# Kernel optimization log

Hardware: AMD Instinct MI355X
Metric: run time of the kernel (lower is better)

Reference implementation:

```python
import jax, jax.numpy as jnp
from jax import lax
import numpy as np

B, W, F, D = 48, 8192, 64, 128  # batch, input_window, c_in, d_model


def setup_inputs() -> dict:
    key = jax.random.key(0)
    k0, k1, k2, k3 = jax.random.split(key, 4)
    x = jax.random.normal(k0, (B, W, F), jnp.float32)
    # ContextConv(c_in->c_in, k=3): conv1d over time, zero 'same' padding (repo layer, assumed standard conv)
    ctx_w = jax.random.normal(k1, (F, F, 3), jnp.float32) * (2.0 / (F * 3)) ** 0.5
    ctx_b = jnp.zeros((F,), jnp.float32)
    # tokenConv: Conv1d(c_in -> d_model, k=3, circular padding, no bias), kaiming fan_in
    token_w = jax.random.normal(k2, (D, F, 3), jnp.float32) * (2.0 / (F * 3)) ** 0.5
    # seW: Linear(c_in -> input_window)
    seW_w = jax.random.normal(k3, (W, F), jnp.float32) * (1.0 / F) ** 0.5
    seW_b = jnp.zeros((W,), jnp.float32)
    return dict(x=x, ctx_w=ctx_w, ctx_b=ctx_b, token_w=token_w, seW_w=seW_w, seW_b=seW_b)


def _conv1d_ncw(x_ncw, w_oiw, padding):
    return lax.conv_general_dilated(
        x_ncw, w_oiw, window_strides=(1,), padding=padding,
        dimension_numbers=("NCW", "OIW", "NCW"))


def reference(x, ctx_w, ctx_b, token_w, seW_w, seW_b):
    # ---- contextConv: (B,W,F) -> (B,W,F), conv over time ----
    xc = _conv1d_ncw(x.transpose(0, 2, 1), ctx_w, [(1, 1)])  # (B,F,W)
    xc = (xc + ctx_b[None, :, None]).transpose(0, 2, 1)       # (B,W,F)

    # ---- structure_embedding (src is detached in torch) ----
    src = lax.stop_gradient(x)
    srcn = src / jnp.linalg.norm(src, axis=-1, keepdims=True)         # row-normalize each timestep
    gram = jnp.einsum('bwf,bwg->bfg', srcn, srcn)                      # batched f x f matmul
    xse = jax.nn.relu(jnp.einsum('bfg,wg->bfw', gram, seW_w) + seW_b[None, None, :])  # (B,F,W)
    xse = xse.transpose(0, 2, 1)                                       # (B,W,F)

    # ---- tokenConv with circular padding ----
    h = (xc + xse).transpose(0, 2, 1)                                  # (B,F,W)
    hp = jnp.pad(h, ((0, 0), (0, 0), (1, 1)), mode='wrap')
    out = _conv1d_ncw(hp, token_w, 'VALID')                            # (B,D,W)
    return out.transpose(0, 2, 1)                                      # (B,W,D)
```

## Files before the change

kernel.cpp:

```cpp
#include <hip/hip_runtime.h>
#include <stdint.h>

#define Bb 48
#define Ww 8192
#define Ff 64
#define Dd 128
#define TWt 64
#define NSLAB 32

#define WS_GRAMP 0u
#define WS_GRAM  25165824u
#define WS_TWT   25952256u
#define WS_CWT   26001408u
#define WS_GBF   26025984u
#define WS_SWB   26419200u
#define WS_XBF   27467776u
#define WS_TOTAL (27467776ull + 50331648ull)

typedef __bf16 bf16x8 __attribute__((ext_vector_type(8)));
typedef float f32x4 __attribute__((ext_vector_type(4)));

__device__ __forceinline__ float bf2f(unsigned short u){
  union { unsigned int i; float f; } v; v.i = ((unsigned int)u) << 16; return v.f;
}
__device__ __forceinline__ unsigned short f2bf(float f){
  union { float f; unsigned int i; } v; v.f = f;
  unsigned int i = v.i;
  return (unsigned short)((i + 0x7fffu + ((i >> 16) & 1u)) >> 16);
}
__device__ __forceinline__ f32x4 mfma16(bf16x8 a, bf16x8 b, f32x4 c){
  return __builtin_amdgcn_mfma_f32_16x16x32_bf16(a, b, c, 0, 0, 0);
}

__device__ __forceinline__ int swz(int row, int col){
  return row * 64 + ((((col >> 3) ^ (row & 7))) << 3) + (col & 7);
}

__global__ __launch_bounds__(256) void prep_weights(const float* __restrict__ ctx_w,
                                                    const float* __restrict__ token_w,
                                                    const float* __restrict__ seW_w,
                                                    unsigned short* __restrict__ cwT,
                                                    unsigned short* __restrict__ twT,
                                                    unsigned short* __restrict__ sWb,
                                                    int fast)
{
  const int bx = blockIdx.x;
  if (bx < 144){
    int idx = bx * 256 + threadIdx.x;
    const int ntw = Dd * 192;
    if (idx < ntw){
      int d = idx / 192, kim = idx % 192;
      int ktap = kim >> 6, fi = kim & 63;
      twT[idx] = f2bf(token_w[(d * Ff + fi) * 3 + ktap]);
    } else if (idx < ntw + Ff * 192){
      int i2 = idx - ntw;
      int f = i2 / 192, kim = i2 % 192;
      int ktap = kim >> 6, fi = kim & 63;
      cwT[i2] = f2bf(ctx_w[(f * Ff + fi) * 3 + ktap]);
    }
  } else if (fast){
    int i = ((bx - 144) * 256 + threadIdx.x) * 8;
    float4 a0 = *(const float4*)(seW_w + i);
    float4 a1 = *(const float4*)(seW_w + i + 4);
    union { uint4 q; unsigned short s[8]; } u;
    u.s[0]=f2bf(a0.x); u.s[1]=f2bf(a0.y); u.s[2]=f2bf(a0.z); u.s[3]=f2bf(a0.w);
    u.s[4]=f2bf(a1.x); u.s[5]=f2bf(a1.y); u.s[6]=f2bf(a1.z); u.s[7]=f2bf(a1.w);
    *(uint4*)(sWb + i) = u.q;
  }
}

__global__ __launch_bounds__(256) void gram_kernel(const float* __restrict__ x,
                                                   unsigned short* __restrict__ xbf,
                                                   float* __restrict__ gramP,
                                                   int writeXbf)
{
  const int b = blockIdx.y;
  const int w_base = blockIdx.x * (Ww / NSLAB);
  const int t = threadIdx.x;
  const int lane = t & 63;
  const int wave = t >> 6;
  const int lrow = lane & 15;
  const int lk = lane >> 4;

  __shared__ unsigned short st[64 * 64];

  f32x4 acc[4] = {};

  const int wl = t >> 2;
  const int f0 = (t & 3) * 16;

  float v[16];
  {
    const float* xr = x + ((size_t)b * Ww + (size_t)(w_base + wl)) * Ff + f0;
    *(float4*)(v)      = *(const float4*)(xr);
    *(float4*)(v + 4)  = *(const float4*)(xr + 4);
    *(float4*)(v + 8)  = *(const float4*)(xr + 8);
    *(float4*)(v + 12) = *(const float4*)(xr + 12);
  }

  for (int sc = 0; sc < 4; ++sc) {
    const size_t rowg = (size_t)b * Ww + (size_t)(w_base + sc * 64 + wl);

    float ss = 0.f;
#pragma unroll
    for (int i = 0; i < 16; ++i) ss += v[i] * v[i];
    ss += __shfl_xor(ss, 1);
    ss += __shfl_xor(ss, 2);
    float rinv = rsqrtf(ss);

    union { uint4 q[2]; unsigned short s[16]; } u;
#pragma unroll
    for (int i = 0; i < 16; ++i){
      u.s[i] = f2bf(v[i]);
      st[swz(f0 + i, wl)] = f2bf(v[i] * rinv);
    }
    if (writeXbf){
      unsigned short* dst = xbf + rowg * Ff + f0;
      *(uint4*)(dst)     = u.q[0];
      *(uint4*)(dst + 8) = u.q[1];
    }

    float vn[16];
    if (sc < 3){
      const float* xr = x + ((size_t)b * Ww + (size_t)(w_base + (sc+1) * 64 + wl)) * Ff + f0;
      *(float4*)(vn)      = *(const float4*)(xr);
      *(float4*)(vn + 4)  = *(const float4*)(xr + 4);
      *(float4*)(vn + 8)  = *(const float4*)(xr + 8);
      *(float4*)(vn + 12) = *(const float4*)(xr + 12);
    }

    __syncthreads();
#pragma unroll
    for (int kc = 0; kc < 2; ++kc){
      const int kw = kc * 32 + lk * 8;
      bf16x8 bfr = *(const bf16x8*)(st + swz(wave * 16 + lrow, kw));
#pragma unroll
      for (int mt = 0; mt < 4; ++mt){
        bf16x8 af = *(const bf16x8*)(st + swz(mt * 16 + lrow, kw));
        acc[mt] = mfma16(af, bfr, acc[mt]);
      }
    }
    __syncthreads();

    if (sc < 3){
#pragma unroll
      for (int i = 0; i < 16; ++i) v[i] = vn[i];
    }
  }

  float* gb = gramP + ((size_t)(blockIdx.x * Bb + b)) * 4096;
#pragma unroll
  for (int mt = 0; mt < 4; ++mt)
#pragma unroll
    for (int r = 0; r < 4; ++r){
      int f = mt * 16 + lk * 4 + r;
      int g = wave * 16 + lrow;
      gb[f * 64 + g] = acc[mt][r];
    }
}

__global__ __launch_bounds__(256) void gram_reduce(const float* __restrict__ gramP,
                                                   float* __restrict__ gram,
                                                   unsigned short* __restrict__ gbf,
                                                   int fast)
{
  int i = blockIdx.x * 256 + threadIdx.x;
  int b = i >> 10;
  int q = i & 1023;
  float sx = 0.f, sy = 0.f, sz = 0.f, sw = 0.f;
#pragma unroll
  for (int sl = 0; sl < NSLAB; ++sl){
    const float4 v = *(const float4*)(gramP + (((size_t)(sl * Bb + b)) << 12) + q * 4);
    sx += v.x; sy += v.y; sz += v.z; sw += v.w;
  }
  float4 s = make_float4(sx, sy, sz, sw);
  *(float4*)(gram + (((size_t)b) << 12) + q * 4) = s;
  if (fast){
    union { unsigned long long u; unsigned short h[4]; } u;
    u.h[0] = f2bf(sx); u.h[1] = f2bf(sy); u.h[2] = f2bf(sz); u.h[3] = f2bf(sw);
    *(unsigned long long*)(gbf + (((size_t)b) << 12) + q * 4) = u.u;
  }
}

__global__ __launch_bounds__(256, 4) void fused_kernel(
    const float* __restrict__ x,
    const unsigned short* __restrict__ xbf,
    const float* __restrict__ ctx_b,
    const float* __restrict__ seW_w,
    const unsigned short* __restrict__ sWb,
    const float* __restrict__ seW_b,
    const float* __restrict__ gram,
    const unsigned short* __restrict__ gbf,
    const unsigned short* __restrict__ cwT,
    const unsigned short* __restrict__ twT,
    float* __restrict__ out,
    int fast)
{
  const int b = blockIdx.y;
  const int w0 = blockIdx.x * TWt;
  const int t = threadIdx.x;
  const int lane = t & 63;
  const int wave = t >> 6;
  const int lrow = lane & 15;
  const int lk = lane >> 4;

  __shared__ __align__(16) unsigned char smem[(84 + 80 + 66) * 64 * 2];
  unsigned short* xs  = (unsigned short*)smem;
  unsigned short* sws = xs + 84 * 64;
  unsigned short* hsh = sws + 80 * 64;

  if (fast){
    for (int item = t; item < 84 * 8; item += 256){
      int i = item >> 3, seg = item & 7;
      int c = w0 - 2 + i;
      uint4 val = make_uint4(0u,0u,0u,0u);
      if (c >= 0 && c < Ww) val = *(const uint4*)(xbf + ((size_t)b*Ww + c)*Ff + seg*8);
      *(uint4*)(xs + swz(i, seg*8)) = val;
    }
    for (int item = t; item < 80 * 8; item += 256){
      int i = item >> 3, seg = item & 7;
      int hc = (w0 - 1 + i) & (Ww - 1);
      *(uint4*)(sws + swz(i, seg*8)) = *(const uint4*)(sWb + (size_t)hc*Ff + seg*8);
    }
  } else {
    for (int item = t; item < 84 * 8; item += 256){
      int i = item >> 3, seg = item & 7;
      int c = w0 - 2 + i;
      union { uint4 q; unsigned short s[8]; } u;
      if (c >= 0 && c < Ww){
        const float* xr = x + ((size_t)b*Ww + c)*Ff + seg*8;
        float4 a0 = *(const float4*)(xr);
        float4 a1 = *(const float4*)(xr + 4);
        u.s[0]=f2bf(a0.x); u.s[1]=f2bf(a0.y); u.s[2]=f2bf(a0.z); u.s[3]=f2bf(a0.w);
        u.s[4]=f2bf(a1.x); u.s[5]=f2bf(a1.y); u.s[6]=f2bf(a1.z); u.s[7]=f2bf(a1.w);
      } else {
        u.q = make_uint4(0u,0u,0u,0u);
      }
      *(uint4*)(xs + swz(i, seg*8)) = u.q;
    }
  }
  __syncthreads();

  const int nt = wave;
  bf16x8 cw_frag[6];
  {
    const unsigned short* p = cwT + (nt*16 + lrow)*192 + lk*8;
#pragma unroll
    for (int kc = 0; kc < 6; ++kc) cw_frag[kc] = *(const bf16x8*)(p + kc*32);
  }
  bf16x8 se_frag[2];
  if (fast){
    const unsigned short* gp = gbf + (size_t)b*4096 + (nt*16 + lrow)*64;
#pragma unroll
    for (int kc = 0; kc < 2; ++kc) se_frag[kc] = *(const bf16x8*)(gp + kc*32 + lk*8);
  } else {
    const float* gb = gram + (size_t)b * 4096;
#pragma unroll
    for (int kc = 0; kc < 2; ++kc){
      union { bf16x8 v; unsigned short s[8]; } u;
#pragma unroll
      for (int j = 0; j < 8; ++j){
        int g = kc*32 + lk*8 + j;
        u.s[j] = f2bf(gb[g*64 + nt*16 + lrow]);
      }
      se_frag[kc] = u.v;
    }
  }

  f32x4 xc_acc[5] = {};
  f32x4 se_acc[5] = {};

#pragma unroll
  for (int mt = 0; mt < 5; ++mt){
#pragma unroll
    for (int kc = 0; kc < 6; ++kc){
      int kim = kc*32 + lk*8;
      int ktap = kim >> 6, fi = kim & 63;
      bf16x8 a = *(const bf16x8*)(xs + swz(mt*16 + lrow + ktap, fi));
      xc_acc[mt] = mfma16(a, cw_frag[kc], xc_acc[mt]);
    }
    if (fast){
#pragma unroll
      for (int kc = 0; kc < 2; ++kc){
        bf16x8 a = *(const bf16x8*)(sws + swz(mt*16 + lrow, kc*32 + lk*8));
        se_acc[mt] = mfma16(a, se_frag[kc], se_acc[mt]);
      }
    } else {
      int hc = (w0 - 1 + mt*16 + lrow) & (Ww - 1);
      const float* sp = seW_w + (size_t)hc * Ff;
#pragma unroll
      for (int kc = 0; kc < 2; ++kc){
        union { bf16x8 v; unsigned short s[8]; } u;
        float4 a0 = *(const float4*)(sp + kc*32 + lk*8);
        float4 a1 = *(const float4*)(sp + kc*32 + lk*8 + 4);
        u.s[0]=f2bf(a0.x); u.s[1]=f2bf(a0.y); u.s[2]=f2bf(a0.z); u.s[3]=f2bf(a0.w);
        u.s[4]=f2bf(a1.x); u.s[5]=f2bf(a1.y); u.s[6]=f2bf(a1.z); u.s[7]=f2bf(a1.w);
        se_acc[mt] = mfma16(u.v, se_frag[kc], se_acc[mt]);
      }
    }
  }

  {
    float cb = ctx_b[nt*16 + lrow];
#pragma unroll
    for (int mt = 0; mt < 5; ++mt){
#pragma unroll
      for (int r = 0; r < 4; ++r){
        int j = mt*16 + lk*4 + r;
        if (j < 66){
          int hc = (w0 - 1 + j) & (Ww - 1);
          float se = se_acc[mt][r] + seW_b[hc];
          se = se > 0.f ? se : 0.f;
          hsh[swz(j, nt*16 + lrow)] = f2bf(xc_acc[mt][r] + cb + se);
        }
      }
    }
  }
  __syncthreads();

  if (blockIdx.x == 0 || blockIdx.x == (Ww/TWt - 1)){
    const int j  = (blockIdx.x == 0) ? 0 : 65;
    const int hc = (blockIdx.x == 0) ? (Ww - 1) : 0;
    if (t < 64){
      const int f = t;
      float a = ctx_b[f];
      for (int ktap = 0; ktap < 3; ++ktap){
        int c = hc + ktap - 1;
        if (c >= 0 && c < Ww){
          const float* xr = x + ((size_t)b*Ww + c)*Ff;
          const unsigned short* wr = cwT + f*192 + ktap*64;
          for (int fi = 0; fi < 64; ++fi) a += xr[fi] * bf2f(wr[fi]);
        }
      }
      const float* gb = gram + (size_t)b * 4096;
      const float* sp = seW_w + (size_t)hc * Ff;
      float se = seW_b[hc];
      for (int g = 0; g < 64; ++g) se += sp[g] * gb[g*64 + f];
      se = se > 0.f ? se : 0.f;
      hsh[swz(j, f)] = f2bf(a + se);
    }
    __syncthreads();
  }

  bf16x8 tw_frag[2][6];
#pragma unroll
  for (int q = 0; q < 2; ++q){
    const unsigned short* p = twT + ((wave*2 + q)*16 + lrow)*192 + lk*8;
#pragma unroll
    for (int kc = 0; kc < 6; ++kc) tw_frag[q][kc] = *(const bf16x8*)(p + kc*32);
  }
  f32x4 oacc[4][2] = {};
#pragma unroll
  for (int mt = 0; mt < 4; ++mt){
#pragma unroll
    for (int kc = 0; kc < 6; ++kc){
      int kim = kc*32 + lk*8;
      int ktap = kim >> 6, fi = kim & 63;
      bf16x8 a = *(const bf16x8*)(hsh + swz(mt*16 + lrow + ktap, fi));
#pragma unroll
      for (int q = 0; q < 2; ++q)
        oacc[mt][q] = mfma16(a, tw_frag[q][kc], oacc[mt][q]);
    }
  }

#pragma unroll
  for (int mt = 0; mt < 4; ++mt){
#pragma unroll
    for (int q = 0; q < 2; ++q)
#pragma unroll
      for (int r = 0; r < 4; ++r){
        int row = w0 + mt*16 + lk*4 + r;
        int d   = (wave*2 + q)*16 + lrow;
        out[((size_t)b*Ww + row)*Dd + d] = oacc[mt][q][r];
      }
  }
}

extern "C" void kernel_launch(void* const* d_in, const int* in_sizes, int n_in,
                              void* d_out, int out_size, void* d_ws, size_t ws_size,
                              hipStream_t stream)
{
  const float* x       = (const float*)d_in[0];
  const float* ctx_w   = (const float*)d_in[1];
  const float* ctx_b   = (const float*)d_in[2];
  const float* token_w = (const float*)d_in[3];
  const float* seW_w   = (const float*)d_in[4];
  const float* seW_b   = (const float*)d_in[5];
  float* out = (float*)d_out;

  char* ws = (char*)d_ws;
  float*          gramP = (float*)(ws + WS_GRAMP);
  float*          gram  = (float*)(ws + WS_GRAM);
  unsigned short* twT   = (unsigned short*)(ws + WS_TWT);
  unsigned short* cwT   = (unsigned short*)(ws + WS_CWT);
  unsigned short* gbf   = (unsigned short*)(ws + WS_GBF);
  unsigned short* sWb   = (unsigned short*)(ws + WS_SWB);
  unsigned short* xbf   = (unsigned short*)(ws + WS_XBF);

  const int fast = (ws_size >= (size_t)WS_TOTAL) ? 1 : 0;

  prep_weights<<<dim3(400), dim3(256), 0, stream>>>(ctx_w, token_w, seW_w, cwT, twT, sWb, fast);
  gram_kernel<<<dim3(NSLAB, Bb), dim3(256), 0, stream>>>(x, xbf, gramP, fast);
  gram_reduce<<<dim3(192), dim3(256), 0, stream>>>(gramP, gram, gbf, fast);
  fused_kernel<<<dim3(Ww/TWt, Bb), dim3(256), 0, stream>>>(
      x, xbf, ctx_b, seW_w, sWb, seW_b, gram, gbf, cwT, twT, out, fast);
}
```

Measured before the change: 362.9 us.

## Process four time tiles per block with register prefetch of next tile

```diff
diff --git a/kernel.cpp b/kernel.cpp
--- a/kernel.cpp
+++ b/kernel.cpp
@@ -6,6 +6,7 @@
 #define Ff 64
 #define Dd 128
 #define TWt 64
+#define TPB 4
 #define NSLAB 32
 
 #define WS_GRAMP 0u
@@ -182,7 +183,7 @@
   }
 }
 
-__global__ __launch_bounds__(256, 4) void fused_kernel(
+__global__ __launch_bounds__(256, 3) void fused_kernel(
     const float* __restrict__ x,
     const unsigned short* __restrict__ xbf,
     const float* __restrict__ ctx_b,
@@ -197,57 +198,31 @@
     int fast)
 {
   const int b = blockIdx.y;
-  const int w0 = blockIdx.x * TWt;
   const int t = threadIdx.x;
   const int lane = t & 63;
   const int wave = t >> 6;
   const int lrow = lane & 15;
   const int lk = lane >> 4;
 
-  __shared__ __align__(16) unsigned char smem[(84 + 80 + 66) * 64 * 2];
-  unsigned short* xs  = (unsigned short*)smem;
-  unsigned short* sws = xs + 84 * 64;
-  unsigned short* hsh = sws + 80 * 64;
-
-  if (fast){
-    for (int item = t; item < 84 * 8; item += 256){
-      int i = item >> 3, seg = item & 7;
-      int c = w0 - 2 + i;
-      uint4 val = make_uint4(0u,0u,0u,0u);
-      if (c >= 0 && c < Ww) val = *(const uint4*)(xbf + ((size_t)b*Ww + c)*Ff + seg*8);
-      *(uint4*)(xs + swz(i, seg*8)) = val;
-    }
-    for (int item = t; item < 80 * 8; item += 256){
-      int i = item >> 3, seg = item & 7;
-      int hc = (w0 - 1 + i) & (Ww - 1);
-      *(uint4*)(sws + swz(i, seg*8)) = *(const uint4*)(sWb + (size_t)hc*Ff + seg*8);
-    }
-  } else {
-    for (int item = t; item < 84 * 8; item += 256){
-      int i = item >> 3, seg = item & 7;
-      int c = w0 - 2 + i;
-      union { uint4 q; unsigned short s[8]; } u;
-      if (c >= 0 && c < Ww){
-        const float* xr = x + ((size_t)b*Ww + c)*Ff + seg*8;
-        float4 a0 = *(const float4*)(xr);
-        float4 a1 = *(const float4*)(xr + 4);
-        u.s[0]=f2bf(a0.x); u.s[1]=f2bf(a0.y); u.s[2]=f2bf(a0.z); u.s[3]=f2bf(a0.w);
-        u.s[4]=f2bf(a1.x); u.s[5]=f2bf(a1.y); u.s[6]=f2bf(a1.z); u.s[7]=f2bf(a1.w);
-      } else {
-        u.q = make_uint4(0u,0u,0u,0u);
-      }
-      *(uint4*)(xs + swz(i, seg*8)) = u.q;
-    }
-  }
-  __syncthreads();
+  __shared__ __align__(16) unsigned short xs[84 * 64];
+  __shared__ __align__(16) unsigned short sws[80 * 64];
+  __shared__ __align__(16) unsigned short hsh[66 * 64];
 
   const int nt = wave;
+
   bf16x8 cw_frag[6];
   {
     const unsigned short* p = cwT + (nt*16 + lrow)*192 + lk*8;
 #pragma unroll
     for (int kc = 0; kc < 6; ++kc) cw_frag[kc] = *(const bf16x8*)(p + kc*32);
   }
+  bf16x8 tw_frag[2][6];
+#pragma unroll
+  for (int q = 0; q < 2; ++q){
+    const unsigned short* p = twT + ((wave*2 + q)*16 + lrow)*192 + lk*8;
+#pragma unroll
+    for (int kc = 0; kc < 6; ++kc) tw_frag[q][kc] = *(const bf16x8*)(p + kc*32);
+  }
   bf16x8 se_frag[2];
   if (fast){
     const unsigned short* gp = gbf + (size_t)b*4096 + (nt*16 + lrow)*64;
@@ -267,112 +242,174 @@
     }
   }
 
-  f32x4 xc_acc[5] = {};
-  f32x4 se_acc[5] = {};
-
-#pragma unroll
-  for (int mt = 0; mt < 5; ++mt){
-#pragma unroll
-    for (int kc = 0; kc < 6; ++kc){
-      int kim = kc*32 + lk*8;
-      int ktap = kim >> 6, fi = kim & 63;
-      bf16x8 a = *(const bf16x8*)(xs + swz(mt*16 + lrow + ktap, fi));
-      xc_acc[mt] = mfma16(a, cw_frag[kc], xc_acc[mt]);
-    }
+  const int w0 = blockIdx.x * (TWt * TPB);
+
+  uint4 xr[3], sr[3];
+  if (fast){
+#pragma unroll
+    for (int k = 0; k < 3; ++k){
+      int item = t + 256*k;
+      if (item < 84*8){
+        int i = item >> 3, seg = item & 7, c = w0 - 2 + i;
+        uint4 val = make_uint4(0u,0u,0u,0u);
+        if (c >= 0 && c < Ww) val = *(const uint4*)(xbf + ((size_t)b*Ww + c)*Ff + seg*8);
+        xr[k] = val;
+      }
+      if (item < 80*8){
+        int i = item >> 3, seg = item & 7, hc = (w0 - 1 + i) & (Ww - 1);
+        sr[k] = *(const uint4*)(sWb + (size_t)hc*Ff + seg*8);
+      }
+    }
+  }
+
+  for (int tt = 0; tt < TPB; ++tt){
+    const int wt = w0 + tt * TWt;
+
     if (fast){
 #pragma unroll
-      for (int kc = 0; kc < 2; ++kc){
-        bf16x8 a = *(const bf16x8*)(sws + swz(mt*16 + lrow, kc*32 + lk*8));
-        se_acc[mt] = mfma16(a, se_frag[kc], se_acc[mt]);
+      for (int k = 0; k < 3; ++k){
+        int item = t + 256*k;
+        if (item < 84*8){ int i = item >> 3, seg = item & 7; *(uint4*)(xs + swz(i, seg*8)) = xr[k]; }
+        if (item < 80*8){ int i = item >> 3, seg = item & 7; *(uint4*)(sws + swz(i, seg*8)) = sr[k]; }
       }
     } else {
-      int hc = (w0 - 1 + mt*16 + lrow) & (Ww - 1);
-      const float* sp = seW_w + (size_t)hc * Ff;
-#pragma unroll
-      for (int kc = 0; kc < 2; ++kc){
-        union { bf16x8 v; unsigned short s[8]; } u;
-        float4 a0 = *(const float4*)(sp + kc*32 + lk*8);
-        float4 a1 = *(const float4*)(sp + kc*32 + lk*8 + 4);
-        u.s[0]=f2bf(a0.x); u.s[1]=f2bf(a0.y); u.s[2]=f2bf(a0.z); u.s[3]=f2bf(a0.w);
-        u.s[4]=f2bf(a1.x); u.s[5]=f2bf(a1.y); u.s[6]=f2bf(a1.z); u.s[7]=f2bf(a1.w);
-        se_acc[mt] = mfma16(u.v, se_frag[kc], se_acc[mt]);
-      }
-    }
-  }
-
-  {
-    float cb = ctx_b[nt*16 + lrow];
+      for (int item = t; item < 84 * 8; item += 256){
+        int i = item >> 3, seg = item & 7;
+        int c = wt - 2 + i;
+        union { uint4 q; unsigned short s[8]; } u;
+        if (c >= 0 && c < Ww){
+          const float* xrp = x + ((size_t)b*Ww + c)*Ff + seg*8;
+          float4 a0 = *(const float4*)(xrp);
+          float4 a1 = *(const float4*)(xrp + 4);
+          u.s[0]=f2bf(a0.x); u.s[1]=f2bf(a0.y); u.s[2]=f2bf(a0.z); u.s[3]=f2bf(a0.w);
+          u.s[4]=f2bf(a1.x); u.s[5]=f2bf(a1.y); u.s[6]=f2bf(a1.z); u.s[7]=f2bf(a1.w);
+        } else {
+          u.q = make_uint4(0u,0u,0u,0u);
+        }
+        *(uint4*)(xs + swz(i, seg*8)) = u.q;
+      }
+    }
+    __syncthreads();
+
+    if (fast && tt + 1 < TPB){
+      const int wn = wt + TWt;
+#pragma unroll
+      for (int k = 0; k < 3; ++k){
+        int item = t + 256*k;
+        if (item < 84*8){
+          int i = item >> 3, seg = item & 7, c = wn - 2 + i;
+          uint4 val = make_uint4(0u,0u,0u,0u);
+          if (c >= 0 && c < Ww) val = *(const uint4*)(xbf + ((size_t)b*Ww + c)*Ff + seg*8);
+          xr[k] = val;
+        }
+        if (item < 80*8){
+          int i = item >> 3, seg = item & 7, hc = (wn - 1 + i) & (Ww - 1);
+          sr[k] = *(const uint4*)(sWb + (size_t)hc*Ff + seg*8);
+        }
+      }
+    }
+
+    f32x4 xc_acc[5] = {};
+    f32x4 se_acc[5] = {};
+
 #pragma unroll
     for (int mt = 0; mt < 5; ++mt){
 #pragma unroll
-      for (int r = 0; r < 4; ++r){
-        int j = mt*16 + lk*4 + r;
-        if (j < 66){
-          int hc = (w0 - 1 + j) & (Ww - 1);
-          float se = se_acc[mt][r] + seW_b[hc];
-          se = se > 0.f ? se : 0.f;
-          hsh[swz(j, nt*16 + lrow)] = f2bf(xc_acc[mt][r] + cb + se);
-        }
-      }
-    }
-  }
-  __syncthreads();
-
-  if (blockIdx.x == 0 || blockIdx.x == (Ww/TWt - 1)){
-    const int j  = (blockIdx.x == 0) ? 0 : 65;
-    const int hc = (blockIdx.x == 0) ? (Ww - 1) : 0;
-    if (t < 64){
-      const int f = t;
-      float a = ctx_b[f];
-      for (int ktap = 0; ktap < 3; ++ktap){
-        int c = hc + ktap - 1;
-        if (c >= 0 && c < Ww){
-          const float* xr = x + ((size_t)b*Ww + c)*Ff;
-          const unsigned short* wr = cwT + f*192 + ktap*64;
-          for (int fi = 0; fi < 64; ++fi) a += xr[fi] * bf2f(wr[fi]);
-        }
-      }
-      const float* gb = gram + (size_t)b * 4096;
-      const float* sp = seW_w + (size_t)hc * Ff;
-      float se = seW_b[hc];
-      for (int g = 0; g < 64; ++g) se += sp[g] * gb[g*64 + f];
-      se = se > 0.f ? se : 0.f;
-      hsh[swz(j, f)] = f2bf(a + se);
+      for (int kc = 0; kc < 6; ++kc){
+        int kim = kc*32 + lk*8;
+        int ktap = kim >> 6, fi = kim & 63;
+        bf16x8 a = *(const bf16x8*)(xs + swz(mt*16 + lrow + ktap, fi));
+        xc_acc[mt] = mfma16(a, cw_frag[kc], xc_acc[mt]);
+      }
+      if (fast){
+#pragma unroll
+        for (int kc = 0; kc < 2; ++kc){
+          bf16x8 a = *(const bf16x8*)(sws + swz(mt*16 + lrow, kc*32 + lk*8));
+          se_acc[mt] = mfma16(a, se_frag[kc], se_acc[mt]);
+        }
+      } else {
+        int hc = (wt - 1 + mt*16 + lrow) & (Ww - 1);
+        const float* sp = seW_w + (size_t)hc * Ff;
+#pragma unroll
+        for (int kc = 0; kc < 2; ++kc){
+          union { bf16x8 v; unsigned short s[8]; } u;
+          float4 a0 = *(const float4*)(sp + kc*32 + lk*8);
+          float4 a1 = *(const float4*)(sp + kc*32 + lk*8 + 4);
+          u.s[0]=f2bf(a0.x); u.s[1]=f2bf(a0.y); u.s[2]=f2bf(a0.z); u.s[3]=f2bf(a0.w);
+          u.s[4]=f2bf(a1.x); u.s[5]=f2bf(a1.y); u.s[6]=f2bf(a1.z); u.s[7]=f2bf(a1.w);
+          se_acc[mt] = mfma16(u.v, se_frag[kc], se_acc[mt]);
+        }
+      }
+    }
+
+    {
+      float cb = ctx_b[nt*16 + lrow];
+#pragma unroll
+      for (int mt = 0; mt < 5; ++mt){
+#pragma unroll
+        for (int r = 0; r < 4; ++r){
+          int j = mt*16 + lk*4 + r;
+          if (j < 66){
+            int hc = (wt - 1 + j) & (Ww - 1);
+            float se = se_acc[mt][r] + seW_b[hc];
+            se = se > 0.f ? se : 0.f;
+            hsh[swz(j, nt*16 + lrow)] = f2bf(xc_acc[mt][r] + cb + se);
+          }
+        }
+      }
     }
     __syncthreads();
-  }
-
-  bf16x8 tw_frag[2][6];
-#pragma unroll
-  for (int q = 0; q < 2; ++q){
-    const unsigned short* p = twT + ((wave*2 + q)*16 + lrow)*192 + lk*8;
-#pragma unroll
-    for (int kc = 0; kc < 6; ++kc) tw_frag[q][kc] = *(const bf16x8*)(p + kc*32);
-  }
-  f32x4 oacc[4][2] = {};
-#pragma unroll
-  for (int mt = 0; mt < 4; ++mt){
-#pragma unroll
-    for (int kc = 0; kc < 6; ++kc){
-      int kim = kc*32 + lk*8;
-      int ktap = kim >> 6, fi = kim & 63;
-      bf16x8 a = *(const bf16x8*)(hsh + swz(mt*16 + lrow + ktap, fi));
+
+    const int tg = blockIdx.x * TPB + tt;
+    if (tg == 0 || tg == (Ww/TWt - 1)){
+      const int j  = (tg == 0) ? 0 : 65;
+      const int hc = (tg == 0) ? (Ww - 1) : 0;
+      if (t < 64){
+        const int f = t;
+        float a = ctx_b[f];
+        for (int ktap = 0; ktap < 3; ++ktap){
+          int c = hc + ktap - 1;
+          if (c >= 0 && c < Ww){
+            const float* xrp = x + ((size_t)b*Ww + c)*Ff;
+            const unsigned short* wr = cwT + f*192 + ktap*64;
+            for (int fi = 0; fi < 64; ++fi) a += xrp[fi] * bf2f(wr[fi]);
+          }
+        }
+        const float* gb = gram + (size_t)b * 4096;
+        const float* sp = seW_w + (size_t)hc * Ff;
+        float se = seW_b[hc];
+        for (int g = 0; g < 64; ++g) se += sp[g] * gb[g*64 + f];
+        se = se > 0.f ? se : 0.f;
+        hsh[swz(j, f)] = f2bf(a + se);
+      }
+      __syncthreads();
+    }
+
+    f32x4 oacc[4][2] = {};
+#pragma unroll
+    for (int mt = 0; mt < 4; ++mt){
+#pragma unroll
+      for (int kc = 0; kc < 6; ++kc){
+        int kim = kc*32 + lk*8;
+        int ktap = kim >> 6, fi = kim & 63;
+        bf16x8 a = *(const bf16x8*)(hsh + swz(mt*16 + lrow + ktap, fi));
+#pragma unroll
+        for (int q = 0; q < 2; ++q)
+          oacc[mt][q] = mfma16(a, tw_frag[q][kc], oacc[mt][q]);
+      }
+    }
+
+#pragma unroll
+    for (int mt = 0; mt < 4; ++mt){
 #pragma unroll
       for (int q = 0; q < 2; ++q)
-        oacc[mt][q] = mfma16(a, tw_frag[q][kc], oacc[mt][q]);
-    }
-  }
-
-#pragma unroll
-  for (int mt = 0; mt < 4; ++mt){
-#pragma unroll
-    for (int q = 0; q < 2; ++q)
-#pragma unroll
-      for (int r = 0; r < 4; ++r){
-        int row = w0 + mt*16 + lk*4 + r;
-        int d   = (wave*2 + q)*16 + lrow;
-        out[((size_t)b*Ww + row)*Dd + d] = oacc[mt][q][r];
-      }
+#pragma unroll
+        for (int r = 0; r < 4; ++r){
+          int row = wt + mt*16 + lk*4 + r;
+          int d   = (wave*2 + q)*16 + lrow;
+          out[((size_t)b*Ww + row)*Dd + d] = oacc[mt][q][r];
+        }
+    }
   }
 }
 
@@ -402,6 +439,6 @@
   prep_weights<<<dim3(400), dim3(256), 0, stream>>>(ctx_w, token_w, seW_w, cwT, twT, sWb, fast);
   gram_kernel<<<dim3(NSLAB, Bb), dim3(256), 0, stream>>>(x, xbf, gramP, fast);
   gram_reduce<<<dim3(192), dim3(256), 0, stream>>>(gramP, gram, gbf, fast);
-  fused_kernel<<<dim3(Ww/TWt, Bb), dim3(256), 0, stream>>>(
+  fused_kernel<<<dim3(Ww/(TWt*TPB), Bb), dim3(256), 0, stream>>>(
       x, xbf, ctx_b, seW_w, sWb, seW_b, gram, gbf, cwT, twT, out, fast);
 }
```

Measured after the change: 575.8 us. 1.59x slower.

## Fold weight prep into gram kernel and widen gram chunks to 128 rows

Applied to the files above, without the earlier changes.

```diff
diff --git a/kernel.cpp b/kernel.cpp
--- a/kernel.cpp
+++ b/kernel.cpp
@@ -35,116 +35,116 @@
 __device__ __forceinline__ int swz(int row, int col){
   return row * 64 + ((((col >> 3) ^ (row & 7))) << 3) + (col & 7);
 }
-
-__global__ __launch_bounds__(256) void prep_weights(const float* __restrict__ ctx_w,
-                                                    const float* __restrict__ token_w,
-                                                    const float* __restrict__ seW_w,
-                                                    unsigned short* __restrict__ cwT,
-                                                    unsigned short* __restrict__ twT,
-                                                    unsigned short* __restrict__ sWb,
-                                                    int fast)
-{
-  const int bx = blockIdx.x;
-  if (bx < 144){
-    int idx = bx * 256 + threadIdx.x;
-    const int ntw = Dd * 192;
-    if (idx < ntw){
-      int d = idx / 192, kim = idx % 192;
-      int ktap = kim >> 6, fi = kim & 63;
-      twT[idx] = f2bf(token_w[(d * Ff + fi) * 3 + ktap]);
-    } else if (idx < ntw + Ff * 192){
-      int i2 = idx - ntw;
-      int f = i2 / 192, kim = i2 % 192;
-      int ktap = kim >> 6, fi = kim & 63;
-      cwT[i2] = f2bf(ctx_w[(f * Ff + fi) * 3 + ktap]);
-    }
-  } else if (fast){
-    int i = ((bx - 144) * 256 + threadIdx.x) * 8;
-    float4 a0 = *(const float4*)(seW_w + i);
-    float4 a1 = *(const float4*)(seW_w + i + 4);
-    union { uint4 q; unsigned short s[8]; } u;
-    u.s[0]=f2bf(a0.x); u.s[1]=f2bf(a0.y); u.s[2]=f2bf(a0.z); u.s[3]=f2bf(a0.w);
-    u.s[4]=f2bf(a1.x); u.s[5]=f2bf(a1.y); u.s[6]=f2bf(a1.z); u.s[7]=f2bf(a1.w);
-    *(uint4*)(sWb + i) = u.q;
-  }
+__device__ __forceinline__ int swzW(int row, int col){
+  return row * 128 + ((((col >> 3) ^ (row & 7))) << 3) + (col & 7);
 }
 
 __global__ __launch_bounds__(256) void gram_kernel(const float* __restrict__ x,
                                                    unsigned short* __restrict__ xbf,
                                                    float* __restrict__ gramP,
-                                                   int writeXbf)
+                                                   const float* __restrict__ ctx_w,
+                                                   const float* __restrict__ token_w,
+                                                   const float* __restrict__ seW_w,
+                                                   unsigned short* __restrict__ cwT,
+                                                   unsigned short* __restrict__ twT,
+                                                   unsigned short* __restrict__ sWb,
+                                                   int fast)
 {
+  if (blockIdx.x >= NSLAB){
+    const int ntw = Dd * 192;
+    const int npack = ntw + Ff * 192;
+    const int nslots = npack + 65536;
+    int vid = ((blockIdx.x - NSLAB) * Bb + blockIdx.y) * 256 + threadIdx.x;
+    const int stride = 2 * Bb * 256;
+    for (; vid < nslots; vid += stride){
+      if (vid < ntw){
+        int d = vid / 192, kim = vid % 192;
+        int ktap = kim >> 6, fi = kim & 63;
+        twT[vid] = f2bf(token_w[(d * Ff + fi) * 3 + ktap]);
+      } else if (vid < npack){
+        int i2 = vid - ntw;
+        int f = i2 / 192, kim = i2 % 192;
+        int ktap = kim >> 6, fi = kim & 63;
+        cwT[i2] = f2bf(ctx_w[(f * Ff + fi) * 3 + ktap]);
+      } else if (fast){
+        int i = (vid - npack) * 8;
+        float4 a0 = *(const float4*)(seW_w + i);
+        float4 a1 = *(const float4*)(seW_w + i + 4);
+        union { uint4 q; unsigned short s[8]; } u;
+        u.s[0]=f2bf(a0.x); u.s[1]=f2bf(a0.y); u.s[2]=f2bf(a0.z); u.s[3]=f2bf(a0.w);
+        u.s[4]=f2bf(a1.x); u.s[5]=f2bf(a1.y); u.s[6]=f2bf(a1.z); u.s[7]=f2bf(a1.w);
+        *(uint4*)(sWb + i) = u.q;
+      }
+    }
+    return;
+  }
+
   const int b = blockIdx.y;
-  const int w_base = blockIdx.x * (Ww / NSLAB);
+  const int w_base = blockIdx.x * 256;
   const int t = threadIdx.x;
   const int lane = t & 63;
   const int wave = t >> 6;
   const int lrow = lane & 15;
   const int lk = lane >> 4;
 
-  __shared__ unsigned short st[64 * 64];
+  __shared__ unsigned short st[64 * 128];
 
   f32x4 acc[4] = {};
 
-  const int wl = t >> 2;
-  const int f0 = (t & 3) * 16;
-
-  float v[16];
+  const int wl = t >> 1;
+  const int f0 = (t & 1) * 32;
+
+  float v[32];
   {
     const float* xr = x + ((size_t)b * Ww + (size_t)(w_base + wl)) * Ff + f0;
-    *(float4*)(v)      = *(const float4*)(xr);
-    *(float4*)(v + 4)  = *(const float4*)(xr + 4);
-    *(float4*)(v + 8)  = *(const float4*)(xr + 8);
-    *(float4*)(v + 12) = *(const float4*)(xr + 12);
-  }
-
-  for (int sc = 0; sc < 4; ++sc) {
-    const size_t rowg = (size_t)b * Ww + (size_t)(w_base + sc * 64 + wl);
+#pragma unroll
+    for (int j = 0; j < 8; ++j) *(float4*)(v + 4*j) = *(const float4*)(xr + 4*j);
+  }
+
+  for (int sc = 0; sc < 2; ++sc) {
+    const size_t rowg = (size_t)b * Ww + (size_t)(w_base + sc * 128 + wl);
 
     float ss = 0.f;
 #pragma unroll
-    for (int i = 0; i < 16; ++i) ss += v[i] * v[i];
+    for (int i = 0; i < 32; ++i) ss += v[i] * v[i];
     ss += __shfl_xor(ss, 1);
-    ss += __shfl_xor(ss, 2);
     float rinv = rsqrtf(ss);
 
-    union { uint4 q[2]; unsigned short s[16]; } u;
-#pragma unroll
-    for (int i = 0; i < 16; ++i){
+    union { uint4 q[4]; unsigned short s[32]; } u;
+#pragma unroll
+    for (int i = 0; i < 32; ++i){
       u.s[i] = f2bf(v[i]);
-      st[swz(f0 + i, wl)] = f2bf(v[i] * rinv);
-    }
-    if (writeXbf){
+      st[swzW(f0 + i, wl)] = f2bf(v[i] * rinv);
+    }
+    if (fast){
       unsigned short* dst = xbf + rowg * Ff + f0;
-      *(uint4*)(dst)     = u.q[0];
-      *(uint4*)(dst + 8) = u.q[1];
-    }
-
-    float vn[16];
-    if (sc < 3){
-      const float* xr = x + ((size_t)b * Ww + (size_t)(w_base + (sc+1) * 64 + wl)) * Ff + f0;
-      *(float4*)(vn)      = *(const float4*)(xr);
-      *(float4*)(vn + 4)  = *(const float4*)(xr + 4);
-      *(float4*)(vn + 8)  = *(const float4*)(xr + 8);
-      *(float4*)(vn + 12) = *(const float4*)(xr + 12);
+#pragma unroll
+      for (int j = 0; j < 4; ++j) *(uint4*)(dst + 8*j) = u.q[j];
+    }
+
+    float vn[32];
+    if (sc == 0){
+      const float* xr = x + ((size_t)b * Ww + (size_t)(w_base + 128 + wl)) * Ff + f0;
+#pragma unroll
+      for (int j = 0; j < 8; ++j) *(float4*)(vn + 4*j) = *(const float4*)(xr + 4*j);
     }
 
     __syncthreads();
 #pragma unroll
-    for (int kc = 0; kc < 2; ++kc){
+    for (int kc = 0; kc < 4; ++kc){
       const int kw = kc * 32 + lk * 8;
-      bf16x8 bfr = *(const bf16x8*)(st + swz(wave * 16 + lrow, kw));
+      bf16x8 bfr = *(const bf16x8*)(st + swzW(wave * 16 + lrow, kw));
 #pragma unroll
       for (int mt = 0; mt < 4; ++mt){
-        bf16x8 af = *(const bf16x8*)(st + swz(mt * 16 + lrow, kw));
+        bf16x8 af = *(const bf16x8*)(st + swzW(mt * 16 + lrow, kw));
         acc[mt] = mfma16(af, bfr, acc[mt]);
       }
     }
     __syncthreads();
 
-    if (sc < 3){
-#pragma unroll
-      for (int i = 0; i < 16; ++i) v[i] = vn[i];
+    if (sc == 0){
+#pragma unroll
+      for (int i = 0; i < 32; ++i) v[i] = vn[i];
     }
   }
 
@@ -399,8 +399,8 @@
 
   const int fast = (ws_size >= (size_t)WS_TOTAL) ? 1 : 0;
 
-  prep_weights<<<dim3(400), dim3(256), 0, stream>>>(ctx_w, token_w, seW_w, cwT, twT, sWb, fast);
-  gram_kernel<<<dim3(NSLAB, Bb), dim3(256), 0, stream>>>(x, xbf, gramP, fast);
+  gram_kernel<<<dim3(NSLAB + 2, Bb), dim3(256), 0, stream>>>(
+      x, xbf, gramP, ctx_w, token_w, seW_w, cwT, twT, sWb, fast);
   gram_reduce<<<dim3(192), dim3(256), 0, stream>>>(gramP, gram, gbf, fast);
   fused_kernel<<<dim3(Ww/TWt, Bb), dim3(256), 0, stream>>>(
       x, xbf, ctx_b, seW_w, sWb, seW_b, gram, gbf, cwT, twT, out, fast);
```

New measurement: 366.3 us. Within noise of the previous version (+1.0%).
